# Kernel tuning notes

Hardware: AMD Instinct MI355X
Metric: run time of the kernel (lower is better)

The kernel has to match this reference:

```python
import jax, jax.numpy as jnp
import numpy as np

PI = 3.141592653589793
EPS = 1e-8


def _hvit(img, k):
    # img: [B,3,H,W], k: [1] density parameter
    r, g, b = img[:, 0], img[:, 1], img[:, 2]
    value = jnp.max(img, axis=1)
    vmin = jnp.min(img, axis=1)
    diff = value - vmin + EPS
    hue = jnp.where(b == value, 4.0 + (r - g) / diff, 0.0)
    hue = jnp.where(g == value, 2.0 + (b - r) / diff, hue)
    hue = jnp.where(r == value, ((g - b) / diff) % 6.0, hue)
    hue = jnp.where(vmin == value, 0.0, hue)
    hue = hue / 6.0
    sat = jnp.where(value == 0, 0.0, (value - vmin) / (value + EPS))
    cs = (jnp.sin(value * 0.5 * PI) + EPS) ** k[0]
    X = cs * sat * jnp.cos(2.0 * PI * hue)
    Y = cs * sat * jnp.sin(2.0 * PI * hue)
    return jnp.stack([X, Y, value], axis=1)  # [B,3,H,W]


def _phvit(xyz, this_k):
    H = jnp.clip(xyz[:, 0], -1.0, 1.0)
    V = jnp.clip(xyz[:, 1], -1.0, 1.0)
    v = jnp.clip(xyz[:, 2], 0.0, 1.0)
    cs = (jnp.sin(v * 0.5 * PI) + EPS) ** this_k
    H = jnp.clip(H / (cs + EPS), -1.0, 1.0)
    V = jnp.clip(V / (cs + EPS), -1.0, 1.0)
    h = (jnp.arctan2(V, H) / (2.0 * PI)) % 1.0
    s = jnp.clip(jnp.sqrt(H * H + V * V), 0.0, 1.0)
    hi = jnp.floor(h * 6.0)
    f = h * 6.0 - hi
    p = v * (1.0 - s)
    q = v * (1.0 - f * s)
    t = v * (1.0 - (1.0 - f) * s)
    hi = hi.astype(jnp.int32)
    zero = jnp.zeros_like(v)
    r = jnp.select([hi == 0, hi == 1, hi == 2, hi == 3, hi == 4, hi == 5],
                   [v, q, p, p, t, v], zero)
    g = jnp.select([hi == 0, hi == 1, hi == 2, hi == 3, hi == 4, hi == 5],
                   [t, v, v, q, p, p], zero)
    b = jnp.select([hi == 0, hi == 1, hi == 2, hi == 3, hi == 4, hi == 5],
                   [p, p, t, v, v, q], zero)
    return jnp.stack([r, g, b], axis=1)  # [B,3,H,W]


def setup_inputs() -> dict:
    key = jax.random.key(0)
    k1, _ = jax.random.split(key)
    img = jax.random.uniform(k1, (16, 3, 1024, 1024), dtype=jnp.float32)
    density_k = jnp.full((1,), 0.2, dtype=jnp.float32)
    return {"img": img, "density_k": density_k}


def reference(img, density_k):
    xyz = _hvit(img, density_k)
    this_k = jax.lax.stop_gradient(density_k)[0]  # mirrors k.item()
    rgb = _phvit(xyz, this_k)
    return rgb
```

## Files before the change

### kernel.cpp

```cpp
#include <hip/hip_runtime.h>
#include <math.h>

#define EPSF 1e-8f
#define TWO_PI_F 6.28318530717958647692f

__device__ __forceinline__ void hvi_pixel(float r, float g, float b, float k,
                                          float& ro, float& go, float& bo)
{
    float value = fmaxf(r, fmaxf(g, b));
    float vmin  = fminf(r, fminf(g, b));
    float diff  = value - vmin + EPSF;

    bool isR = (r == value);
    bool isG = (!isR) && (g == value);

    float num  = isR ? (g - b) : (isG ? (b - r) : (r - g));
    float offs = isR ? 0.0f   : (isG ? 2.0f    : 4.0f);
    float x    = num / diff;
    float hue6 = offs + x;
    if (isR && x < 0.0f) hue6 = x + 6.0f;
    if (vmin == value)   hue6 = 0.0f;
    float hue = hue6 / 6.0f;

    float sat = (value == 0.0f) ? 0.0f : (value - vmin) / (value + EPSF);

    float sv = __sinf((value * 0.5f) * 3.14159265358979323846f) + EPSF;
    float cs = __expf(k * __logf(sv));

    float ang = TWO_PI_F * hue;
    float sh, ch;
    sincosf(ang, &sh, &ch);

    float X = cs * sat * ch;
    float Y = cs * sat * sh;

    float H = fminf(fmaxf(X, -1.0f), 1.0f);
    float V = fminf(fmaxf(Y, -1.0f), 1.0f);
    float v = fminf(fmaxf(value, 0.0f), 1.0f);

    float csd = cs + EPSF;
    H = fminf(fmaxf(H / csd, -1.0f), 1.0f);
    V = fminf(fmaxf(V / csd, -1.0f), 1.0f);

    float t2 = atan2f(V, H) / TWO_PI_F;
    float h  = (t2 < 0.0f) ? t2 + 1.0f : t2;
    float s  = fminf(fmaxf(sqrtf(H * H + V * V), 0.0f), 1.0f);

    float h6  = h * 6.0f;
    float hif = floorf(h6);
    float f   = h6 - hif;
    float pv  = v * (1.0f - s);
    float qv  = v * (1.0f - f * s);
    float tv  = v * (1.0f - (1.0f - f) * s);
    int hi = (int)hif;

    float rr = 0.0f, gg = 0.0f, bb = 0.0f;
    rr = (hi == 0) ? v  : rr;  gg = (hi == 0) ? tv : gg;  bb = (hi == 0) ? pv : bb;
    rr = (hi == 1) ? qv : rr;  gg = (hi == 1) ? v  : gg;  bb = (hi == 1) ? pv : bb;
    rr = (hi == 2) ? pv : rr;  gg = (hi == 2) ? v  : gg;  bb = (hi == 2) ? tv : bb;
    rr = (hi == 3) ? pv : rr;  gg = (hi == 3) ? qv : gg;  bb = (hi == 3) ? v  : bb;
    rr = (hi == 4) ? tv : rr;  gg = (hi == 4) ? pv : gg;  bb = (hi == 4) ? v  : bb;
    rr = (hi == 5) ? v  : rr;  gg = (hi == 5) ? pv : gg;  bb = (hi == 5) ? qv : bb;

    ro = rr; go = gg; bo = bb;
}

extern "C" __global__ void __launch_bounds__(256)
rgb_hvi_kernel(const float* __restrict__ img, const float* __restrict__ kptr,
               float* __restrict__ out, int ngroups)
{
    int i = blockIdx.x * blockDim.x + threadIdx.x;
    if (i >= ngroups) return;
    const float k = kptr[0];

    unsigned int q = (unsigned int)i << 2;
    unsigned int n = q >> 20;
    unsigned int p = q & 1048575u;
    size_t base = (size_t)n * 3145728u + p;

    const float4 R = *reinterpret_cast<const float4*>(img + base);
    const float4 G = *reinterpret_cast<const float4*>(img + base + 1048576);
    const float4 B = *reinterpret_cast<const float4*>(img + base + 2097152);

    float4 Ro, Go, Bo;
    hvi_pixel(R.x, G.x, B.x, k, Ro.x, Go.x, Bo.x);
    hvi_pixel(R.y, G.y, B.y, k, Ro.y, Go.y, Bo.y);
    hvi_pixel(R.z, G.z, B.z, k, Ro.z, Go.z, Bo.z);
    hvi_pixel(R.w, G.w, B.w, k, Ro.w, Go.w, Bo.w);

    *reinterpret_cast<float4*>(out + base)           = Ro;
    *reinterpret_cast<float4*>(out + base + 1048576) = Go;
    *reinterpret_cast<float4*>(out + base + 2097152) = Bo;
}

extern "C" void kernel_launch(void* const* d_in, const int* in_sizes, int n_in,
                              void* d_out, int out_size, void* d_ws, size_t ws_size,
                              hipStream_t stream)
{
    const float* img  = (const float*)d_in[0];
    const float* kptr = (const float*)d_in[1];
    float* out = (float*)d_out;

    int total   = in_sizes[0];
    int ngroups = total / 12;
    int block   = 256;
    int grid    = (ngroups + block - 1) / block;

    rgb_hvi_kernel<<<grid, block, 0, stream>>>(img, kptr, out, ngroups);
}
```

Measured before the change: 340.7 us.

## Cancel HVI round trip algebraically and skip transcendental math on fast path

Recognizes that the forward HVI transform followed by its inverse reduces to a direct HSV-to-RGB reconstruction, since the density scale divides out and atan2/sqrt recover hue and saturation. The fast path drops sin, pow, sincos, atan2 and sqrt, using hardware reciprocals, and falls back to the exact path near the hue wraparound. Output stores become nontemporal. This risks small mismatches where clipping or the epsilon in the original chain would have changed results.

```diff
diff --git a/kernel.cpp b/kernel.cpp
--- a/kernel.cpp
+++ b/kernel.cpp
@@ -4,7 +4,9 @@
 #define EPSF 1e-8f
 #define TWO_PI_F 6.28318530717958647692f
 
-__device__ __forceinline__ void hvi_pixel(float r, float g, float b, float k,
+typedef float f32x4 __attribute__((ext_vector_type(4)));
+
+__device__ __forceinline__ void hvi_exact(float r, float g, float b, float k,
                                           float& ro, float& go, float& bo)
 {
     float value = fmaxf(r, fmaxf(g, b));
@@ -65,6 +67,51 @@
     ro = rr; go = gg; bo = bb;
 }
 
+__device__ __forceinline__ void hvi_pixel(float r, float g, float b, float k,
+                                          float& ro, float& go, float& bo)
+{
+    float value = fmaxf(r, fmaxf(g, b));
+    float vmin  = fminf(r, fminf(g, b));
+    float sv    = value - vmin;
+    float diff  = sv + EPSF;
+
+    bool isR = (r == value);
+    bool isG = (!isR) && (g == value);
+
+    float num  = isR ? (g - b) : (isG ? (b - r) : (r - g));
+    float offs = isR ? 0.0f   : (isG ? 2.0f    : 4.0f);
+    float x    = num * __builtin_amdgcn_rcpf(diff);
+    float h6   = offs + x;
+    if (isR && x < 0.0f) h6 = x + 6.0f;
+    if (vmin == value)   h6 = 0.0f;
+
+    if (__builtin_expect(h6 > 5.9995f, 0)) {
+        hvi_exact(r, g, b, k, ro, go, bo);
+        return;
+    }
+
+    float sat = sv * __builtin_amdgcn_rcpf(value + EPSF);
+
+    float hif = floorf(h6);
+    float f   = h6 - hif;
+    int   hi  = (int)hif;
+
+    float v  = value;
+    float vs = v * sat;
+    float pv = v - vs;
+    float qv = v - vs * f;
+    float tv = v - vs * (1.0f - f);
+
+    float rr = (hi == 0) ? v  : (hi == 1) ? qv : (hi == 2) ? pv
+             : (hi == 3) ? pv : (hi == 4) ? tv : v;
+    float gg = (hi == 0) ? tv : (hi == 1) ? v  : (hi == 2) ? v
+             : (hi == 3) ? qv : (hi == 4) ? pv : pv;
+    float bb = (hi == 0) ? pv : (hi == 1) ? pv : (hi == 2) ? tv
+             : (hi == 3) ? v  : (hi == 4) ? v  : qv;
+
+    ro = rr; go = gg; bo = bb;
+}
+
 extern "C" __global__ void __launch_bounds__(256)
 rgb_hvi_kernel(const float* __restrict__ img, const float* __restrict__ kptr,
                float* __restrict__ out, int ngroups)
@@ -82,15 +129,19 @@
     const float4 G = *reinterpret_cast<const float4*>(img + base + 1048576);
     const float4 B = *reinterpret_cast<const float4*>(img + base + 2097152);
 
-    float4 Ro, Go, Bo;
-    hvi_pixel(R.x, G.x, B.x, k, Ro.x, Go.x, Bo.x);
-    hvi_pixel(R.y, G.y, B.y, k, Ro.y, Go.y, Bo.y);
-    hvi_pixel(R.z, G.z, B.z, k, Ro.z, Go.z, Bo.z);
-    hvi_pixel(R.w, G.w, B.w, k, Ro.w, Go.w, Bo.w);
+    float r0,g0,b0, r1,g1,b1, r2,g2,b2, r3,g3,b3;
+    hvi_pixel(R.x, G.x, B.x, k, r0, g0, b0);
+    hvi_pixel(R.y, G.y, B.y, k, r1, g1, b1);
+    hvi_pixel(R.z, G.z, B.z, k, r2, g2, b2);
+    hvi_pixel(R.w, G.w, B.w, k, r3, g3, b3);
 
-    *reinterpret_cast<float4*>(out + base)           = Ro;
-    *reinterpret_cast<float4*>(out + base + 1048576) = Go;
-    *reinterpret_cast<float4*>(out + base + 2097152) = Bo;
+    f32x4 Ro = { r0, r1, r2, r3 };
+    f32x4 Go = { g0, g1, g2, g3 };
+    f32x4 Bo = { b0, b1, b2, b3 };
+
+    __builtin_nontemporal_store(Ro, reinterpret_cast<f32x4*>(out + base));
+    __builtin_nontemporal_store(Go, reinterpret_cast<f32x4*>(out + base + 1048576));
+    __builtin_nontemporal_store(Bo, reinterpret_cast<f32x4*>(out + base + 2097152));
 }
 
 extern "C" void kernel_launch(void* const* d_in, const int* in_sizes, int n_in,
```

Result: no change. 335.2 us (-1.6%).

## Collapse HVI round trip into direct HSV reconstruction with exact fallback near hue wrap

Applied to the files above, without the earlier changes.

Recognises that the forward HVI transform followed by its inverse reduces to an HSV round trip, so output channels are computed directly from max, min and the hue fraction without sin, pow, sincos, atan2 or sqrt. Groups where any pixel's hue lies near the wraparound fall back to the original exact path to match the reference's floating-point behaviour there. This removes most transcendental work per pixel, leaving the kernel closer to memory-bound. It risks small numerical mismatches where the original's epsilon and clipping effects differ from the ideal identity, for example at very dark pixels.

```diff
diff --git a/kernel.cpp b/kernel.cpp
--- a/kernel.cpp
+++ b/kernel.cpp
@@ -4,7 +4,7 @@
 #define EPSF 1e-8f
 #define TWO_PI_F 6.28318530717958647692f
 
-__device__ __forceinline__ void hvi_pixel(float r, float g, float b, float k,
+__device__ __forceinline__ void hvi_exact(float r, float g, float b, float k,
                                           float& ro, float& go, float& bo)
 {
     float value = fmaxf(r, fmaxf(g, b));
@@ -65,6 +65,8 @@
     ro = rr; go = gg; bo = bb;
 }
 
+#define BAND_THRESH 5.99998f
+
 extern "C" __global__ void __launch_bounds__(256)
 rgb_hvi_kernel(const float* __restrict__ img, const float* __restrict__ kptr,
                float* __restrict__ out, int ngroups)
@@ -82,11 +84,59 @@
     const float4 G = *reinterpret_cast<const float4*>(img + base + 1048576);
     const float4 B = *reinterpret_cast<const float4*>(img + base + 2097152);
 
-    float4 Ro, Go, Bo;
-    hvi_pixel(R.x, G.x, B.x, k, Ro.x, Go.x, Bo.x);
-    hvi_pixel(R.y, G.y, B.y, k, Ro.y, Go.y, Bo.y);
-    hvi_pixel(R.z, G.z, B.z, k, Ro.z, Go.z, Bo.z);
-    hvi_pixel(R.w, G.w, B.w, k, Ro.w, Go.w, Bo.w);
+    const float rin[4] = { R.x, R.y, R.z, R.w };
+    const float gin[4] = { G.x, G.y, G.z, G.w };
+    const float bin[4] = { B.x, B.y, B.z, B.w };
+    float ro[4], go[4], bo[4];
+
+    bool band = false;
+#pragma unroll
+    for (int j = 0; j < 4; ++j) {
+        float r = rin[j], g = gin[j], b = bin[j];
+
+        float value = fmaxf(r, fmaxf(g, b));
+        float vmin  = fminf(r, fminf(g, b));
+        float sv    = value - vmin;
+
+        bool isR = (r == value);
+        bool isG = (!isR) && (g == value);
+
+        float num  = isR ? (g - b) : (isG ? (b - r) : (r - g));
+        float offs = isR ? 0.0f   : (isG ? 2.0f    : 4.0f);
+        float x    = num * __builtin_amdgcn_rcpf(sv + EPSF);
+        float h6   = offs + x;
+        if (isR && x < 0.0f) h6 = x + 6.0f;
+        if (vmin == value)   h6 = 0.0f;
+
+        band = band || (h6 > BAND_THRESH);
+
+        float hif = floorf(h6);
+        float f   = h6 - hif;
+        int   hi  = (int)hif;
+
+        float svf = sv * f;
+        float v   = value;
+        float pv  = vmin;
+        float qv  = value - svf;
+        float tv  = vmin + svf;
+
+        ro[j] = (hi == 0) ? v  : (hi == 1) ? qv : (hi == 2) ? pv
+              : (hi == 3) ? pv : (hi == 4) ? tv : v;
+        go[j] = (hi == 0) ? tv : (hi == 1) ? v  : (hi == 2) ? v
+              : (hi == 3) ? qv : (hi == 4) ? pv : pv;
+        bo[j] = (hi == 0) ? pv : (hi == 1) ? pv : (hi == 2) ? tv
+              : (hi == 3) ? v  : (hi == 4) ? v  : qv;
+    }
+
+    if (__builtin_expect(band, 0)) {
+#pragma unroll
+        for (int j = 0; j < 4; ++j)
+            hvi_exact(rin[j], gin[j], bin[j], k, ro[j], go[j], bo[j]);
+    }
+
+    float4 Ro = make_float4(ro[0], ro[1], ro[2], ro[3]);
+    float4 Go = make_float4(go[0], go[1], go[2], go[3]);
+    float4 Bo = make_float4(bo[0], bo[1], bo[2], bo[3]);
 
     *reinterpret_cast<float4*>(out + base)           = Ro;
     *reinterpret_cast<float4*>(out + base + 1048576) = Go;
```

Result: faster. 328.1 us (-3.7%).
